# Optimization experiments

Hardware: AMD Instinct MI355X
Metric: run time of the kernel (lower is better)

Reference implementation:

```python
import jax, jax.numpy as jnp
import numpy as np

N, E, H, D_IN, D_HID, D_OUT = 50000, 800000, 2, 128, 64, 16
NEG_SLOPE = 0.2


def leaky(x, slope=NEG_SLOPE):
    return jnp.where(x >= 0, x, slope * x)


def gatv2_layer(x, src, dst, W_src, W_dst, attn, bias):
    # x: [N, Fin]; W_src/W_dst: [Fin, H*D]; attn: [H, D]; bias: [H*D]
    fs = (x @ W_src).reshape(-1, H, D_HID)  # source projection [N,H,D]
    fd = (x @ W_dst).reshape(-1, H, D_HID)  # dest projection   [N,H,D]
    e = leaky(fs[src] + fd[dst])             # [E,H,D] GATv2: LeakyReLU before attn dot
    logits = jnp.einsum('ehd,hd->eh', e, attn)  # [E,H]
    # edge softmax over incoming edges of each dst node
    m = jax.ops.segment_max(logits, dst, num_segments=N)  # [N,H]
    a = jnp.exp(logits - m[dst])
    s = jax.ops.segment_sum(a, dst, num_segments=N)       # [N,H]
    alpha = a / s[dst]                                     # [E,H]
    msg = fs[src] * alpha[..., None]                       # [E,H,D]
    out = jax.ops.segment_sum(msg, dst, num_segments=N)   # [N,H,D]
    return out.reshape(N, H * D_HID) + bias


def setup_inputs() -> dict:
    key = jax.random.key(0)
    ks = jax.random.split(key, 12)
    sc = 0.05
    return {
        'x': jax.random.normal(ks[0], (N, D_IN), jnp.float32),
        'src': jax.random.randint(ks[1], (E,), 0, N),
        'dst': jax.random.randint(ks[2], (E,), 0, N),
        'Wsrc0': jax.random.normal(ks[3], (D_IN, H * D_HID), jnp.float32) * sc,
        'Wdst0': jax.random.normal(ks[4], (D_IN, H * D_HID), jnp.float32) * sc,
        'attn0': jax.random.normal(ks[5], (H, D_HID), jnp.float32) * sc,
        'bias0': jnp.zeros((H * D_HID,), jnp.float32),
        'Wsrc1': jax.random.normal(ks[6], (H * D_HID, H * D_HID), jnp.float32) * sc,
        'Wdst1': jax.random.normal(ks[7], (H * D_HID, H * D_HID), jnp.float32) * sc,
        'attn1': jax.random.normal(ks[8], (H, D_HID), jnp.float32) * sc,
        'bias1': jnp.zeros((H * D_HID,), jnp.float32),
        'R0W': jax.random.normal(ks[9], (D_IN, D_OUT), jnp.float32) * sc,
        'R0b': jnp.zeros((D_OUT,), jnp.float32),
        'R1W': jax.random.normal(ks[10], (H * D_HID, D_OUT), jnp.float32) * sc,
        'R1b': jnp.zeros((D_OUT,), jnp.float32),
        'R2W': jax.random.normal(ks[11], (H * D_HID, D_OUT), jnp.float32) * sc,
        'R2b': jnp.zeros((D_OUT,), jnp.float32),
    }


def reference(x, src, dst, Wsrc0, Wdst0, attn0, bias0, Wsrc1, Wdst1, attn1, bias1,
              R0W, R0b, R1W, R1b, R2W, R2b):
    # eval mode: all dropouts / edge-drop are identity; norm='none'
    h0 = x
    h1 = leaky(gatv2_layer(h0, src, dst, Wsrc0, Wdst0, attn0, bias0))
    h2 = leaky(gatv2_layer(h1, src, dst, Wsrc1, Wdst1, attn1, bias1))
    # jumping-knowledge readout: sum of per-layer linear readouts
    score = (h0 @ R0W + R0b) + (h1 @ R1W + R1b) + (h2 @ R2W + R2b)
    return score
```

## Files before the change

kernel.cpp:

```cpp
#include <hip/hip_runtime.h>

#define NN 50000
#define NNP 50048
#define NE 800000
#define DF 128
#define BCAP 64
#define NCHUNK (NE / 256)
#define HB_PER_RANGE 512
#define HF_BLOCKS (HB_PER_RANGE * 8)
#define PROJ_BLOCKS ((NN + 63) / 64)

typedef __attribute__((ext_vector_type(8))) short short8v;
typedef __attribute__((ext_vector_type(4))) float float4v;
typedef __attribute__((ext_vector_type(2))) _Float16 half2v;

__device__ __forceinline__ float leaky(float t) { return fmaxf(t, 0.2f * t); }

__device__ __forceinline__ unsigned short rne_bf16(float x) {
  unsigned u = __float_as_uint(x);
  u = (u + 0x7fffu + ((u >> 16) & 1u)) >> 16;
  return (unsigned short)u;
}

template <int CTRL>
__device__ __forceinline__ float dpp_add(float v) {
  const int i = __builtin_bit_cast(int, v);
  const int p = __builtin_amdgcn_update_dpp(0, i, CTRL, 0xF, 0xF, true);
  return v + __builtin_bit_cast(float, p);
}
__device__ __forceinline__ float reduce8_dpp(float v) {
  v = dpp_add<0xB1>(v);
  v = dpp_add<0x4E>(v);
  v = dpp_add<0x141>(v);
  return v;
}

__global__ void prep_kernel(int* __restrict__ deg,
                            const float* __restrict__ Ws0, const float* __restrict__ Wd0,
                            const float* __restrict__ Ws1, const float* __restrict__ Wd1,
                            unsigned short* __restrict__ WT0, unsigned short* __restrict__ WT1,
                            const float* __restrict__ R0W, const float* __restrict__ R1W,
                            const float* __restrict__ R2W, unsigned short* __restrict__ RT) {
  const int b = blockIdx.x;
  const int tid = threadIdx.x;
  if (b < 196) {
    const int i = b * 256 + tid;
    if (i < NN) deg[i] = 0;
  } else if (b < 452) {
    const int idx = (b - 196) * 256 + tid;
    const int l = idx >> 15;
    const int r = (idx >> 7) & 255;
    const int k = idx & 127;
    const float* Ws = l ? Ws1 : Ws0;
    const float* Wd = l ? Wd1 : Wd0;
    const float v = (r < 128) ? Ws[k * DF + r] : Wd[k * DF + (r - 128)];
    (l ? WT1 : WT0)[r * DF + k] = rne_bf16(v);
  } else {
    const int idx = (b - 452) * 256 + tid;
    const int c = idx / 384, k = idx - c * 384;
    const float* Rw = (k < 128) ? R0W : (k < 256) ? R1W : R2W;
    RT[c * 384 + k] = rne_bf16(Rw[(k & 127) * 16 + c]);
  }
}

template <bool L0>
__device__ __forceinline__ void proj_body(unsigned short (*At)[136], int blk, int tid,
                                          const unsigned short* __restrict__ Ab,
                                          const float* __restrict__ Xf,
                                          unsigned short* __restrict__ XbOut,
                                          const unsigned short* __restrict__ WT,
                                          _Float16* __restrict__ fsh,
                                          _Float16* __restrict__ fdh) {
  const int w = tid >> 6, l = tid & 63;

#pragma unroll
  for (int i = 0; i < 4; ++i) {
    const int flat = i * 256 + tid;
    const int r = flat >> 4, c16 = flat & 15;
    const int row = blk * 64 + r;
    uint4 v = make_uint4(0, 0, 0, 0);
    if (L0) {
      if (row < NN) {
        const float4 a = ((const float4*)Xf)[row * 32 + c16 * 2];
        const float4 bq = ((const float4*)Xf)[row * 32 + c16 * 2 + 1];
        v.x = rne_bf16(a.x) | ((unsigned)rne_bf16(a.y) << 16);
        v.y = rne_bf16(a.z) | ((unsigned)rne_bf16(a.w) << 16);
        v.z = rne_bf16(bq.x) | ((unsigned)rne_bf16(bq.y) << 16);
        v.w = rne_bf16(bq.z) | ((unsigned)rne_bf16(bq.w) << 16);
        ((uint4*)XbOut)[row * 16 + c16] = v;
      }
    } else {
      if (row < NN) v = ((const uint4*)Ab)[row * 16 + c16];
    }
    *(uint4*)&At[r][c16 * 8] = v;
  }

  const int kof = (l >> 4) * 8;
  const int cbase = w * 64 + (l & 15);
  short8v b[4][4];
#pragma unroll
  for (int ct = 0; ct < 4; ++ct)
#pragma unroll
    for (int kk = 0; kk < 4; ++kk)
      b[ct][kk] = *(const short8v*)(WT + (cbase + ct * 16) * DF + kk * 32 + kof);
  __syncthreads();

  const int lrow = l & 15;
#pragma unroll
  for (int rt = 0; rt < 4; ++rt) {
    short8v a[4];
#pragma unroll
    for (int kk = 0; kk < 4; ++kk) a[kk] = *(const short8v*)&At[rt * 16 + lrow][kk * 32 + kof];
    const int r0 = blk * 64 + rt * 16 + (l >> 4) * 4;
#pragma unroll
    for (int ct = 0; ct < 4; ++ct) {
      float4v acc = {0.f, 0.f, 0.f, 0.f};
#pragma unroll
      for (int kk = 0; kk < 4; ++kk)
        acc = __builtin_amdgcn_mfma_f32_16x16x32_bf16(a[kk], b[ct][kk], acc, 0, 0, 0);
      const int col = cbase + ct * 16;
      _Float16* O = (col < DF) ? fsh : fdh;
      const int c2 = (col < DF) ? col : col - DF;
#pragma unroll
      for (int r = 0; r < 4; ++r)
        if (r0 + r < NN) O[(r0 + r) * DF + c2] = (_Float16)acc[r];
    }
  }
}

__global__ __launch_bounds__(256) void stage1_kernel(
    const int* __restrict__ src, const int* __restrict__ dst, int* __restrict__ deg,
    unsigned short* __restrict__ ssrcB, const float* __restrict__ Xf,
    unsigned short* __restrict__ XbOut, const unsigned short* __restrict__ WT0,
    _Float16* __restrict__ fsh, _Float16* __restrict__ fdh) {
  __shared__ unsigned short At[64][136];
  const int b = blockIdx.x;
  const int tid = threadIdx.x;
  if (b >= PROJ_BLOCKS) {
    const int range = b & 7;
    const int rlo = range * 6250, rhi = rlo + 6250;
    const int hb = b - PROJ_BLOCKS;
    for (int c = hb >> 3; c < NCHUNK; c += HB_PER_RANGE) {
      const int e = c * 256 + tid;
      const int dn = dst[e];
      const int sv = src[e];
      if (dn >= rlo && dn < rhi) {
        const int k = atomicAdd(&deg[dn], 1);
        if (k < BCAP) ssrcB[dn * BCAP + k] = (unsigned short)sv;
      }
    }
    return;
  }
  proj_body<true>(At, b, tid, nullptr, Xf, XbOut, WT0, fsh, fdh);
}

__global__ __launch_bounds__(256) void proj_mfma_kernel(const unsigned short* __restrict__ Ab,
                                                        const unsigned short* __restrict__ WT,
                                                        _Float16* __restrict__ fsh,
                                                        _Float16* __restrict__ fdh) {
  __shared__ unsigned short At[64][136];
  proj_body<false>(At, blockIdx.x, threadIdx.x, Ab, nullptr, nullptr, WT, fsh, fdh);
}

__global__ __launch_bounds__(256) void csr_attention_kernel(
    const _Float16* __restrict__ fsh, const _Float16* __restrict__ fdh,
    const float* __restrict__ attn, const int* __restrict__ degv,
    const unsigned short* __restrict__ ssrcB, const float* __restrict__ bias,
    unsigned short* __restrict__ houtb) {
  const int node = (blockIdx.x * 256 + threadIdx.x) >> 6;
  const int lane = threadIdx.x & 63;
  const int eg = lane >> 4, s16 = lane & 15;
  const int deg = min(degv[node], BCAP);
  const unsigned short* __restrict__ sb = ssrcB + node * BCAP;
  const uint4* __restrict__ fsh4 = (const uint4*)fsh;

  half2v fdv[4], at[4];
  {
    const uint4 fq = ((const uint4*)fdh)[node * 16 + s16];
    fdv[0] = __builtin_bit_cast(half2v, fq.x);
    fdv[1] = __builtin_bit_cast(half2v, fq.y);
    fdv[2] = __builtin_bit_cast(half2v, fq.z);
    fdv[3] = __builtin_bit_cast(half2v, fq.w);
    const float4 a0 = ((const float4*)(attn + s16 * 8))[0];
    const float4 a1 = ((const float4*)(attn + s16 * 8))[1];
    const float l2e = 1.44269504f;
    at[0] = (half2v){(_Float16)(a0.x * l2e), (_Float16)(a0.y * l2e)};
    at[1] = (half2v){(_Float16)(a0.z * l2e), (_Float16)(a0.w * l2e)};
    at[2] = (half2v){(_Float16)(a1.x * l2e), (_Float16)(a1.y * l2e)};
    at[3] = (half2v){(_Float16)(a1.z * l2e), (_Float16)(a1.w * l2e)};
  }
  const half2v c02 = {(_Float16)0.2f, (_Float16)0.2f};

  float s = 0.f;
  half2v acc[4] = {{0, 0}, {0, 0}, {0, 0}, {0, 0}};
  const int nfull = deg >> 2;
  const int rem = deg & 3;

  auto consume = [&](const uint4 q) {
    half2v f[4];
    f[0] = __builtin_bit_cast(half2v, q.x);
    f[1] = __builtin_bit_cast(half2v, q.y);
    f[2] = __builtin_bit_cast(half2v, q.z);
    f[3] = __builtin_bit_cast(half2v, q.w);
    float v = 0.f;
#pragma unroll
    for (int k = 0; k < 4; ++k) {
      const half2v t = f[k] + fdv[k];
      const half2v lk = __builtin_elementwise_max(t, t * c02);
      v = __builtin_amdgcn_fdot2(lk, at[k], v, false);
    }
    v = reduce8_dpp(v);
    const float p = exp2f(v);
    s += p;
    const _Float16 ph = (_Float16)p;
    const half2v p2 = {ph, ph};
#pragma unroll
    for (int k = 0; k < 4; ++k) acc[k] = p2 * f[k] + acc[k];
  };

  int snA = (int)sb[eg];
  int snB = (int)sb[eg + 4];
  uint4 qA = fsh4[snA * 16 + s16];
  uint4 qB = fsh4[snB * 16 + s16];
  snA = (int)sb[eg + 8];
  snB = (int)sb[eg + 12];

  int base = eg + 16;
  const int npairs = nfull >> 1;
  for (int jj = 0; jj < npairs; ++jj) {
    consume(qA);
    qA = fsh4[snA * 16 + s16];
    snA = (int)sb[base];
    consume(qB);
    qB = fsh4[snB * 16 + s16];
    snB = (int)sb[base + 4];
    base += 8;
  }
  if (nfull & 1) {
    consume(qA);
    qA = qB;
  }
  if (rem) {
    half2v f[4];
    f[0] = __builtin_bit_cast(half2v, qA.x);
    f[1] = __builtin_bit_cast(half2v, qA.y);
    f[2] = __builtin_bit_cast(half2v, qA.z);
    f[3] = __builtin_bit_cast(half2v, qA.w);
    float v = 0.f;
#pragma unroll
    for (int k = 0; k < 4; ++k) {
      const half2v t = f[k] + fdv[k];
      const half2v lk = __builtin_elementwise_max(t, t * c02);
      v = __builtin_amdgcn_fdot2(lk, at[k], v, false);
    }
    v = reduce8_dpp(v);
    const float p = (eg < rem) ? exp2f(v) : 0.f;
    s += p;
    const _Float16 ph = (_Float16)p;
    const half2v p2 = {ph, ph};
#pragma unroll
    for (int k = 0; k < 4; ++k) acc[k] = p2 * f[k] + acc[k];
  }

#pragma unroll
  for (int dist = 16; dist <= 32; dist <<= 1) {
    s += __shfl_xor(s, dist);
#pragma unroll
    for (int k = 0; k < 4; ++k) {
      const float of = __shfl_xor(__builtin_bit_cast(float, acc[k]), dist);
      acc[k] = acc[k] + __builtin_bit_cast(half2v, of);
    }
  }

  if (lane < 16) {
    const float rs = (deg > 0) ? 1.0f / s : 0.0f;
    const float4 b0 = ((const float4*)(bias + s16 * 8))[0];
    const float4 b1 = ((const float4*)(bias + s16 * 8))[1];
    const float bb[8] = {b0.x, b0.y, b0.z, b0.w, b1.x, b1.y, b1.z, b1.w};
    float ob[8];
#pragma unroll
    for (int k = 0; k < 4; ++k) {
      ob[2 * k]     = leaky(fmaf((float)acc[k].x, rs, bb[2 * k]));
      ob[2 * k + 1] = leaky(fmaf((float)acc[k].y, rs, bb[2 * k + 1]));
    }
    uint4 w;
    w.x = rne_bf16(ob[0]) | ((unsigned)rne_bf16(ob[1]) << 16);
    w.y = rne_bf16(ob[2]) | ((unsigned)rne_bf16(ob[3]) << 16);
    w.z = rne_bf16(ob[4]) | ((unsigned)rne_bf16(ob[5]) << 16);
    w.w = rne_bf16(ob[6]) | ((unsigned)rne_bf16(ob[7]) << 16);
    ((uint4*)houtb)[node * 16 + s16] = w;
  }
}

__global__ __launch_bounds__(256) void readout_mfma_kernel(
    const unsigned short* __restrict__ h0b, const unsigned short* __restrict__ h1b,
    const unsigned short* __restrict__ h2b, const unsigned short* __restrict__ RT,
    const float* __restrict__ R0b, const float* __restrict__ R1b,
    const float* __restrict__ R2b, float* __restrict__ out) {
  const int w = threadIdx.x >> 6, l = threadIdx.x & 63;
  const int row0 = blockIdx.x * 64 + w * 16;
  const int m = l & 15, ksub = (l >> 4) * 8;
  float4v acc = {0.f, 0.f, 0.f, 0.f};
  const unsigned short* hs[3] = {h0b, h1b, h2b};
#pragma unroll
  for (int a = 0; a < 3; ++a) {
    const unsigned short* __restrict__ H = hs[a];
#pragma unroll
    for (int kk = 0; kk < 4; ++kk) {
      const short8v av = *(const short8v*)(H + (size_t)(row0 + m) * DF + kk * 32 + ksub);
      const short8v bv = *(const short8v*)(RT + m * 384 + a * 128 + kk * 32 + ksub);
      acc = __builtin_amdgcn_mfma_f32_16x16x32_bf16(av, bv, acc, 0, 0, 0);
    }
  }
  const float rb = R0b[m] + R1b[m] + R2b[m];
  const int r0 = row0 + (l >> 4) * 4;
#pragma unroll
  for (int r = 0; r < 4; ++r)
    if (r0 + r < NN) out[(r0 + r) * 16 + m] = acc[r] + rb;
}

extern "C" void kernel_launch(void* const* d_in, const int* in_sizes, int n_in,
                              void* d_out, int out_size, void* d_ws, size_t ws_size,
                              hipStream_t stream) {
  const float* x     = (const float*)d_in[0];
  const int*   src   = (const int*)d_in[1];
  const int*   dst   = (const int*)d_in[2];
  const float* Wsrc0 = (const float*)d_in[3];
  const float* Wdst0 = (const float*)d_in[4];
  const float* attn0 = (const float*)d_in[5];
  const float* bias0 = (const float*)d_in[6];
  const float* Wsrc1 = (const float*)d_in[7];
  const float* Wdst1 = (const float*)d_in[8];
  const float* attn1 = (const float*)d_in[9];
  const float* bias1 = (const float*)d_in[10];
  const float* R0W   = (const float*)d_in[11];
  const float* R0b   = (const float*)d_in[12];
  const float* R1W   = (const float*)d_in[13];
  const float* R1b   = (const float*)d_in[14];
  const float* R2W   = (const float*)d_in[15];
  const float* R2b   = (const float*)d_in[16];
  float* out = (float*)d_out;

  unsigned short* xb  = (unsigned short*)d_ws;
  unsigned short* h1b = xb + (size_t)NNP * DF;
  unsigned short* h2b = h1b + (size_t)NNP * DF;
  _Float16* fsh = (_Float16*)(h2b + (size_t)NNP * DF);
  _Float16* fdh = fsh + (size_t)NN * DF;
  unsigned short* WT0 = (unsigned short*)(fdh + (size_t)NN * DF);
  unsigned short* WT1 = WT0 + 256 * DF;
  unsigned short* RT  = WT1 + 256 * DF;
  int* deg = (int*)(RT + 16 * 384);
  unsigned short* ssrcB = (unsigned short*)(deg + NN);

  prep_kernel<<<476, 256, 0, stream>>>(deg, Wsrc0, Wdst0, Wsrc1, Wdst1, WT0, WT1,
                                       R0W, R1W, R2W, RT);

  stage1_kernel<<<PROJ_BLOCKS + HF_BLOCKS, 256, 0, stream>>>(
      src, dst, deg, ssrcB, x, xb, WT0, fsh, fdh);

  csr_attention_kernel<<<(NN * 64) / 256, 256, 0, stream>>>(fsh, fdh, attn0, deg, ssrcB, bias0, h1b);
  proj_mfma_kernel<<<PROJ_BLOCKS, 256, 0, stream>>>(h1b, WT1, fsh, fdh);
  csr_attention_kernel<<<(NN * 64) / 256, 256, 0, stream>>>(fsh, fdh, attn1, deg, ssrcB, bias1, h2b);

  readout_mfma_kernel<<<NNP / 64, 256, 0, stream>>>(xb, h1b, h2b, RT, R0b, R1b, R2b, out);
}
```

Measured before the change: 151.3 us.

## Split readout: fold h0/h1 readout into layer-1 projection launch, halve histogram blocks

The jumping-knowledge readout is split in two. The h0 and h1 contributions are computed by extra blocks in the layer-1 projection kernel, overlapping with the projection work, and the final small kernel only adds the h2 term into the output with a read-modify-write. The number of edge-bucketing blocks per dst range is also halved. The aim is to shorten the critical tail and reduce launch and occupancy overhead. In exchange the output is written twice and read once more.

```diff
diff --git a/kernel.cpp b/kernel.cpp
--- a/kernel.cpp
+++ b/kernel.cpp
@@ -6,7 +6,7 @@
 #define DF 128
 #define BCAP 64
 #define NCHUNK (NE / 256)
-#define HB_PER_RANGE 512
+#define HB_PER_RANGE 256
 #define HF_BLOCKS (HB_PER_RANGE * 8)
 #define PROJ_BLOCKS ((NN + 63) / 64)
 
@@ -128,6 +128,45 @@
   }
 }
 
+template <bool AFIRST>
+__device__ __forceinline__ void readout_body(int blk, int tid,
+                                             const unsigned short* __restrict__ h0b,
+                                             const unsigned short* __restrict__ h1b,
+                                             const unsigned short* __restrict__ h2b,
+                                             const unsigned short* __restrict__ RT,
+                                             const float* __restrict__ R0b,
+                                             const float* __restrict__ R1b,
+                                             const float* __restrict__ R2b,
+                                             float* __restrict__ out) {
+  const int w = tid >> 6, l = tid & 63;
+  const int row0 = blk * 64 + w * 16;
+  const int m = l & 15, ksub = (l >> 4) * 8;
+  float4v acc = {0.f, 0.f, 0.f, 0.f};
+  const unsigned short* hs[3] = {h0b, h1b, h2b};
+  const int a0 = AFIRST ? 0 : 2, a1 = AFIRST ? 2 : 3;
+#pragma unroll
+  for (int a = a0; a < a1; ++a) {
+    const unsigned short* __restrict__ H = hs[a];
+#pragma unroll
+    for (int kk = 0; kk < 4; ++kk) {
+      const short8v av = *(const short8v*)(H + (size_t)(row0 + m) * DF + kk * 32 + ksub);
+      const short8v bv = *(const short8v*)(RT + m * 384 + a * 128 + kk * 32 + ksub);
+      acc = __builtin_amdgcn_mfma_f32_16x16x32_bf16(av, bv, acc, 0, 0, 0);
+    }
+  }
+  const int r0 = row0 + (l >> 4) * 4;
+  if (AFIRST) {
+    const float rb = R0b[m] + R1b[m] + R2b[m];
+#pragma unroll
+    for (int r = 0; r < 4; ++r)
+      if (r0 + r < NN) out[(r0 + r) * 16 + m] = acc[r] + rb;
+  } else {
+#pragma unroll
+    for (int r = 0; r < 4; ++r)
+      if (r0 + r < NN) out[(r0 + r) * 16 + m] += acc[r];
+  }
+}
+
 __global__ __launch_bounds__(256) void stage1_kernel(
     const int* __restrict__ src, const int* __restrict__ dst, int* __restrict__ deg,
     unsigned short* __restrict__ ssrcB, const float* __restrict__ Xf,
@@ -154,12 +193,27 @@
   proj_body<true>(At, b, tid, nullptr, Xf, XbOut, WT0, fsh, fdh);
 }
 
-__global__ __launch_bounds__(256) void proj_mfma_kernel(const unsigned short* __restrict__ Ab,
-                                                        const unsigned short* __restrict__ WT,
-                                                        _Float16* __restrict__ fsh,
-                                                        _Float16* __restrict__ fdh) {
+__global__ __launch_bounds__(256) void projl1_rd01_kernel(
+    const unsigned short* __restrict__ h1b, const unsigned short* __restrict__ WT,
+    _Float16* __restrict__ fsh, _Float16* __restrict__ fdh,
+    const unsigned short* __restrict__ xb, const unsigned short* __restrict__ RT,
+    const float* __restrict__ R0b, const float* __restrict__ R1b,
+    const float* __restrict__ R2b, float* __restrict__ out) {
   __shared__ unsigned short At[64][136];
-  proj_body<false>(At, blockIdx.x, threadIdx.x, Ab, nullptr, nullptr, WT, fsh, fdh);
+  const int b = blockIdx.x;
+  if (b < PROJ_BLOCKS) {
+    proj_body<false>(At, b, threadIdx.x, h1b, nullptr, nullptr, WT, fsh, fdh);
+  } else {
+    readout_body<true>(b - PROJ_BLOCKS, threadIdx.x, xb, h1b, nullptr, RT,
+                       R0b, R1b, R2b, out);
+  }
+}
+
+__global__ __launch_bounds__(256) void readout2_kernel(
+    const unsigned short* __restrict__ h2b, const unsigned short* __restrict__ RT,
+    float* __restrict__ out) {
+  readout_body<false>(blockIdx.x, threadIdx.x, nullptr, nullptr, h2b, RT,
+                      nullptr, nullptr, nullptr, out);
 }
 
 __global__ __launch_bounds__(256) void csr_attention_kernel(
@@ -290,33 +344,6 @@
     w.w = rne_bf16(ob[6]) | ((unsigned)rne_bf16(ob[7]) << 16);
     ((uint4*)houtb)[node * 16 + s16] = w;
   }
-}
-
-__global__ __launch_bounds__(256) void readout_mfma_kernel(
-    const unsigned short* __restrict__ h0b, const unsigned short* __restrict__ h1b,
-    const unsigned short* __restrict__ h2b, const unsigned short* __restrict__ RT,
-    const float* __restrict__ R0b, const float* __restrict__ R1b,
-    const float* __restrict__ R2b, float* __restrict__ out) {
-  const int w = threadIdx.x >> 6, l = threadIdx.x & 63;
-  const int row0 = blockIdx.x * 64 + w * 16;
-  const int m = l & 15, ksub = (l >> 4) * 8;
-  float4v acc = {0.f, 0.f, 0.f, 0.f};
-  const unsigned short* hs[3] = {h0b, h1b, h2b};
-#pragma unroll
-  for (int a = 0; a < 3; ++a) {
-    const unsigned short* __restrict__ H = hs[a];
-#pragma unroll
-    for (int kk = 0; kk < 4; ++kk) {
-      const short8v av = *(const short8v*)(H + (size_t)(row0 + m) * DF + kk * 32 + ksub);
-      const short8v bv = *(const short8v*)(RT + m * 384 + a * 128 + kk * 32 + ksub);
-      acc = __builtin_amdgcn_mfma_f32_16x16x32_bf16(av, bv, acc, 0, 0, 0);
-    }
-  }
-  const float rb = R0b[m] + R1b[m] + R2b[m];
-  const int r0 = row0 + (l >> 4) * 4;
-#pragma unroll
-  for (int r = 0; r < 4; ++r)
-    if (r0 + r < NN) out[(r0 + r) * 16 + m] = acc[r] + rb;
 }
 
 extern "C" void kernel_launch(void* const* d_in, const int* in_sizes, int n_in,
@@ -359,8 +386,11 @@
       src, dst, deg, ssrcB, x, xb, WT0, fsh, fdh);
 
   csr_attention_kernel<<<(NN * 64) / 256, 256, 0, stream>>>(fsh, fdh, attn0, deg, ssrcB, bias0, h1b);
-  proj_mfma_kernel<<<PROJ_BLOCKS, 256, 0, stream>>>(h1b, WT1, fsh, fdh);
+
+  projl1_rd01_kernel<<<2 * PROJ_BLOCKS, 256, 0, stream>>>(
+      h1b, WT1, fsh, fdh, xb, RT, R0b, R1b, R2b, out);
+
   csr_attention_kernel<<<(NN * 64) / 256, 256, 0, stream>>>(fsh, fdh, attn1, deg, ssrcB, bias1, h2b);
 
-  readout_mfma_kernel<<<NNP / 64, 256, 0, stream>>>(xb, h1b, h2b, RT, R0b, R1b, R2b, out);
-}
+  readout2_kernel<<<NNP / 64, 256, 0, stream>>>(h2b, RT, out);
+}
```

New measurement: 147.3 us. 1.03x faster.
